# Kernel tuning notes

Measured on AMD Instinct MI355X. Metric: run time of the kernel, lower is better.

The kernel has to match this reference:

```python
import jax, jax.numpy as jnp
import numpy as np

EPS = 1e-7

def _sample_project(feat, pid, w1, b1, w2, b2):
    # feat: [B, C, H, W]; pid: [P] flat spatial indices into H*W
    B, C, H, W = feat.shape
    fr = jnp.transpose(feat, (0, 2, 3, 1)).reshape(B, H * W, C)  # [B, HW, C]
    x = fr[:, pid, :].reshape(B * pid.shape[0], C)               # gather -> [B*P, C]
    x = jnp.maximum(x @ w1 + b1, 0.0) @ w2 + b2                  # 2-layer MLP
    norm = jnp.sqrt(jnp.sum(x * x, axis=1, keepdims=True))       # L2 over channels
    return x / (norm + EPS)


def setup_inputs() -> dict:
    key = jax.random.key(0)
    ks = jax.random.split(key, 16)
    NC = 256
    shapes = [(16, 256, 128, 128), (16, 512, 64, 64), (16, 1024, 32, 32)]
    inp = {}
    for i, s in enumerate(shapes):
        inp[f"feat{i}"] = jax.random.normal(ks[i], s, dtype=jnp.float32)
        hw = s[2] * s[3]
        inp[f"patch_id{i}"] = jax.random.randint(ks[3 + i], (256,), 0, hw, dtype=jnp.int64)
        C = s[1]
        g = 0.02  # init_gain (normal init)
        inp[f"w1_{i}"] = g * jax.random.normal(ks[6 + 3 * i], (C, NC), dtype=jnp.float32)
        inp[f"b1_{i}"] = jnp.zeros((NC,), dtype=jnp.float32)
        inp[f"w2_{i}"] = g * jax.random.normal(ks[7 + 3 * i], (NC, NC), dtype=jnp.float32)
        inp[f"b2_{i}"] = jnp.zeros((NC,), dtype=jnp.float32)
    return inp


def reference(feat0, feat1, feat2, patch_id0, patch_id1, patch_id2,
              w1_0, b1_0, w2_0, b2_0,
              w1_1, b1_1, w2_1, b2_1,
              w1_2, b1_2, w2_2, b2_2):
    out0 = _sample_project(feat0, patch_id0, w1_0, b1_0, w2_0, b2_0)
    out1 = _sample_project(feat1, patch_id1, w1_1, b1_1, w2_1, b2_1)
    out2 = _sample_project(feat2, patch_id2, w1_2, b1_2, w2_2, b2_2)
    return (out0, out1, out2)
```

## Files before the change

### kernel.cpp

```cpp
#include <hip/hip_runtime.h>

typedef __attribute__((ext_vector_type(8))) short short8;
typedef __attribute__((ext_vector_type(4))) float floatx4;
typedef __attribute__((ext_vector_type(4))) unsigned int uintx4;

__device__ __forceinline__ short f2bf(float f) {
    unsigned u = __builtin_bit_cast(unsigned, f);
    u = (u + 0x7FFFu + ((u >> 16) & 1u)) >> 16;
    return (short)u;
}


__global__ __launch_bounds__(256) void sort_pid(
    const int* __restrict__ pid0, const int* __restrict__ pid1, const int* __restrict__ pid2,
    unsigned short* __restrict__ wsb)
{
    __shared__ int ks[256];
    __shared__ int vs[256];
    const int* pid = (blockIdx.x == 0) ? pid0 : (blockIdx.x == 1) ? pid1 : pid2;
    int t = threadIdx.x;
    ks[t] = pid[t];
    vs[t] = t;
    __syncthreads();
    for (int k = 2; k <= 256; k <<= 1) {
        for (int j = k >> 1; j > 0; j >>= 1) {
            int ixj = t ^ j;
            if (ixj > t) {
                int a = ks[t], b = ks[ixj];
                bool asc = ((t & k) == 0);
                if (asc ? (a > b) : (a < b)) {
                    ks[t] = b; ks[ixj] = a;
                    int va = vs[t]; vs[t] = vs[ixj]; vs[ixj] = va;
                }
            }
            __syncthreads();
        }
    }
    int2* sp = (int2*)(wsb + 7995392) + blockIdx.x * 256;
    sp[t] = make_int2(ks[t], vs[t]);
}

__global__ __launch_bounds__(256) void gather_prep(
    const float* __restrict__ feat0, const float* __restrict__ feat1, const float* __restrict__ feat2,
    const float* __restrict__ w10, const float* __restrict__ w11, const float* __restrict__ w12,
    const float* __restrict__ w20, const float* __restrict__ w21, const float* __restrict__ w22,
    unsigned short* __restrict__ wsb)
{
    __shared__ float tile[32][33];
    int blk = blockIdx.x;
    int t = threadIdx.x;

    if (blk < 640) {
        const float* in; unsigned short* out; int K, t0;
        if (blk < 64)       { in = w10; out = wsb;          K = 256;  t0 = 0; }
        else if (blk < 192) { in = w11; out = wsb + 65536;  K = 512;  t0 = 64; }
        else if (blk < 448) { in = w12; out = wsb + 196608; K = 1024; t0 = 192; }
        else if (blk < 512) { in = w20; out = wsb + 458752; K = 256;  t0 = 448; }
        else if (blk < 576) { in = w21; out = wsb + 524288; K = 256;  t0 = 512; }
        else                { in = w22; out = wsb + 589824; K = 256;  t0 = 576; }
        int tile_id = blk - t0;
        int tk = K >> 5;
        int k0 = (tile_id % tk) << 5;
        int n0 = (tile_id / tk) << 5;
        int j = t & 31, i0 = (t >> 5) << 2;
        #pragma unroll
        for (int u = 0; u < 4; u++)
            tile[i0 + u][j] = in[(size_t)(k0 + i0 + u) * 256 + (n0 + j)];
        __syncthreads();
        int kf = t & 31, nf0 = (t >> 5) << 2;
        #pragma unroll
        for (int u = 0; u < 4; u++)
            out[(size_t)(n0 + nf0 + u) * K + (k0 + kf)] = (unsigned short)f2bf(tile[kf][nf0 + u]);
        return;
    }

    blk -= 640;
    const float* feat; const int2* sp; unsigned short* xg;
    int lblk, cl8, HW, n;
    const int2* spb = (const int2*)(wsb + 7995392);
    if (blk < 512)       { feat = feat0; sp = spb;       lblk = blk;        cl8 = 5; HW = 16384; n = 512;  xg = wsb + 655360; }
    else if (blk < 1536) { feat = feat1; sp = spb + 256; lblk = blk - 512;  cl8 = 6; HW = 4096;  n = 1024; xg = wsb + 1703936; }
    else                 { feat = feat2; sp = spb + 512; lblk = blk - 1536; cl8 = 7; HW = 1024;  n = 2048; xg = wsb + 3801088; }

    lblk = (lblk & 7) * (n >> 3) + (lblk >> 3);

    int g   = (lblk << 8) + t;
    int row = g >> cl8;
    int gk  = (g & ((1 << cl8) - 1)) << 3;
    int b = row >> 8, pp = row & 255;
    int2 e = sp[pp];
    int s = e.x, op = e.y;
    int C = 8 << cl8;

    const float* gp = feat + (size_t)b * ((size_t)C * HW) + (size_t)gk * HW + s;
    float v[8];
    #pragma unroll
    for (int j = 0; j < 8; j++) v[j] = gp[(size_t)j * HW];
    short8 sv;
    #pragma unroll
    for (int j = 0; j < 8; j++) sv[j] = f2bf(v[j]);
    *(short8*)(xg + (size_t)(b * 256 + op) * C + gk) = sv;
}

__global__ __launch_bounds__(256, 2) void fused_mlp(
    const float* __restrict__ b1_0, const float* __restrict__ b1_1, const float* __restrict__ b1_2,
    const float* __restrict__ b2_0, const float* __restrict__ b2_1, const float* __restrict__ b2_2,
    const unsigned short* __restrict__ wsb,
    float* __restrict__ out)
{
    __shared__ __align__(16) unsigned short smem[26944];
    unsigned short* wsS = smem;
    unsigned short* xs  = smem + 18432;
    unsigned short* hs  = smem + 18432;
    float* rs = (float*)(smem + 26880);

    int blk = blockIdx.x;
    int scale = 2 - (blk >> 7);
    int mblk = blk & 127;

    const float* b1; const float* b2;
    const unsigned short* w1T; const unsigned short* w2T; const unsigned short* xg;
    int C; size_t outBase;
    if (scale == 0) { b1 = b1_0; b2 = b2_0; w1T = wsb;          w2T = wsb + 458752;
                      xg = wsb + 655360;  C = 256;  outBase = 0; }
    else if (scale == 1) { b1 = b1_1; b2 = b2_1; w1T = wsb + 65536;  w2T = wsb + 524288;
                      xg = wsb + 1703936; C = 512;  outBase = 1048576; }
    else            { b1 = b1_2; b2 = b2_2; w1T = wsb + 196608; w2T = wsb + 589824;
                      xg = wsb + 3801088; C = 1024; outBase = 2097152; }

    int t = threadIdx.x;
    int wid = t >> 6, lane = t & 63, quad = lane >> 4, l15 = lane & 15;
    int r0 = (wid & 1) << 4;
    int c0 = (wid >> 1) << 7;

    int gr = t >> 3;
    int gk = (t & 7) << 3;
    int row_g = (mblk << 5) + gr;
    const unsigned short* xrow = xg + (size_t)row_g * C;

    floatx4 acc[8];
    #pragma unroll
    for (int f = 0; f < 8; f++) acc[f] = (floatx4){0.f, 0.f, 0.f, 0.f};

    for (int kc = 0; kc < C; kc += 64) {
        *(short8*)(xs + gr * 72 + gk) = *(const short8*)(xrow + kc + gk);
        {
            const uintx4* src = (const uintx4*)(w1T + (size_t)t * C + kc);
            uintx4* dst = (uintx4*)(wsS + t * 72);
            #pragma unroll
            for (int j2 = 0; j2 < 8; j2++) dst[j2] = src[j2];
        }
        __syncthreads();
        const unsigned short* aRow = xs + (r0 + l15) * 72;
        const unsigned short* bRow = wsS + (c0 + l15) * 72;
        #pragma unroll
        for (int ks = 0; ks < 2; ks++) {
            short8 af = *(const short8*)(aRow + ks * 32 + quad * 8);
            #pragma unroll
            for (int f = 0; f < 8; f++) {
                short8 bf = *(const short8*)(bRow + f * (16 * 72) + ks * 32 + quad * 8);
                acc[f] = __builtin_amdgcn_mfma_f32_16x16x32_bf16(af, bf, acc[f], 0, 0, 0);
            }
        }
        __syncthreads();
    }

    {
        float bias1[8];
        #pragma unroll
        for (int f = 0; f < 8; f++) bias1[f] = b1[c0 + f * 16 + l15];
        #pragma unroll
        for (int f = 0; f < 8; f++)
            #pragma unroll
            for (int reg = 0; reg < 4; reg++) {
                float h = fmaxf(acc[f][reg] + bias1[f], 0.f);
                hs[(r0 + quad * 4 + reg) * 264 + (c0 + f * 16 + l15)] = (unsigned short)f2bf(h);
            }
    }

    #pragma unroll
    for (int f = 0; f < 8; f++) acc[f] = (floatx4){0.f, 0.f, 0.f, 0.f};
    const unsigned short* hA = hs + (r0 + l15) * 264;
    for (int kc = 0; kc < 256; kc += 64) {
        {
            const uintx4* src = (const uintx4*)(w2T + (size_t)t * 256 + kc);
            uintx4* dst = (uintx4*)(wsS + t * 72);
            #pragma unroll
            for (int j2 = 0; j2 < 8; j2++) dst[j2] = src[j2];
        }
        __syncthreads();
        const unsigned short* bRow = wsS + (c0 + l15) * 72;
        #pragma unroll
        for (int ks = 0; ks < 2; ks++) {
            short8 af = *(const short8*)(hA + kc + ks * 32 + quad * 8);
            #pragma unroll
            for (int f = 0; f < 8; f++) {
                short8 bf = *(const short8*)(bRow + f * (16 * 72) + ks * 32 + quad * 8);
                acc[f] = __builtin_amdgcn_mfma_f32_16x16x32_bf16(af, bf, acc[f], 0, 0, 0);
            }
        }
        __syncthreads();
    }

    {
        float bias2[8];
        #pragma unroll
        for (int f = 0; f < 8; f++) bias2[f] = b2[c0 + f * 16 + l15];
        float psq[4] = {0.f, 0.f, 0.f, 0.f};
        #pragma unroll
        for (int f = 0; f < 8; f++)
            #pragma unroll
            for (int reg = 0; reg < 4; reg++) {
                float yv = acc[f][reg] + bias2[f];
                acc[f][reg] = yv;
                psq[reg] += yv * yv;
            }
        #pragma unroll
        for (int m = 1; m < 16; m <<= 1)
            #pragma unroll
            for (int reg = 0; reg < 4; reg++)
                psq[reg] += __shfl_xor(psq[reg], m, 16);

        if (t < 32) rs[t] = 0.f;
        __syncthreads();
        if (l15 == 0) {
            #pragma unroll
            for (int reg = 0; reg < 4; reg++)
                atomicAdd(&rs[r0 + quad * 4 + reg], psq[reg]);
        }
        __syncthreads();

        #pragma unroll
        for (int f = 0; f < 8; f++)
            #pragma unroll
            for (int reg = 0; reg < 4; reg++) {
                int row = r0 + quad * 4 + reg;
                float inv = 1.f / (sqrtf(rs[row]) + 1e-7f);
                out[outBase + (size_t)((mblk << 5) + row) * 256 + (c0 + f * 16 + l15)] =
                    acc[f][reg] * inv;
            }
    }
}

extern "C" void kernel_launch(void* const* d_in, const int* in_sizes, int n_in,
                              void* d_out, int out_size, void* d_ws, size_t ws_size,
                              hipStream_t stream)
{
    (void)n_in; (void)out_size; (void)ws_size;
    bool dict = (in_sizes[1] == 256);
    const float *feat[3], *w1[3], *b1[3], *w2[3], *b2[3];
    const int* pid[3];
    for (int i = 0; i < 3; i++) {
        if (dict) {
            feat[i] = (const float*)d_in[i * 6 + 0];
            pid[i]  = (const int*)  d_in[i * 6 + 1];
            w1[i]   = (const float*)d_in[i * 6 + 2];
            b1[i]   = (const float*)d_in[i * 6 + 3];
            w2[i]   = (const float*)d_in[i * 6 + 4];
            b2[i]   = (const float*)d_in[i * 6 + 5];
        } else {
            feat[i] = (const float*)d_in[i];
            pid[i]  = (const int*)  d_in[3 + i];
            w1[i]   = (const float*)d_in[6 + 4 * i + 0];
            b1[i]   = (const float*)d_in[6 + 4 * i + 1];
            w2[i]   = (const float*)d_in[6 + 4 * i + 2];
            b2[i]   = (const float*)d_in[6 + 4 * i + 3];
        }
    }
    unsigned short* wsb = (unsigned short*)d_ws;
    sort_pid<<<3, 256, 0, stream>>>(pid[0], pid[1], pid[2], wsb);
    gather_prep<<<4224, 256, 0, stream>>>(feat[0], feat[1], feat[2],
                                          w1[0], w1[1], w1[2],
                                          w2[0], w2[1], w2[2], wsb);
    fused_mlp<<<384, 256, 0, stream>>>(b1[0], b1[1], b1[2],
                                       b2[0], b2[1], b2[2],
                                       wsb, (float*)d_out);
}
```

Measured before the change: 533.0 us.

## Restructure feature gather to use sorted-patch coalescing and LDS transpose

Reworks the gather stage so each block handles one batch and a 64-channel group. Lanes read consecutive sorted patch positions within each channel plane, and the results are staged as bf16 in a shared-memory tile. The tile is then transposed and written out as contiguous 16-byte row chunks. The aim is better locality on the strided NCHW gather: sorted indices bring nearby spatial reads together and each block reuses its index set. In exchange there are far fewer blocks, a larger shared-memory footprint, and an extra barrier.

New measurement: 521.9 us. 2.1% less time.

```diff
diff --git a/kernel.cpp b/kernel.cpp
--- a/kernel.cpp
+++ b/kernel.cpp
@@ -40,17 +40,59 @@
     sp[t] = make_int2(ks[t], vs[t]);
 }
 
+template<int NCH>
+__device__ __forceinline__ void gather_body(
+    const float* __restrict__ featb, const int2* __restrict__ sp,
+    unsigned short* __restrict__ xg, int C, int HW, int b, int cg, int sh,
+    unsigned short (*tile)[256], int t)
+{
+    int wid = t >> 6, lane = t & 63;
+    int s0 = sh * 128;
+    int sj[NCH];
+    #pragma unroll
+    for (int j = 0; j < NCH; ++j) sj[j] = sp[s0 + j * 64 + lane].x;
+
+    int cbase = cg * 64 + wid * 16;
+    #pragma unroll 2
+    for (int cl = 0; cl < 16; ++cl) {
+        const float* plane = featb + (size_t)(cbase + cl) * HW;
+        float v[NCH];
+        #pragma unroll
+        for (int j = 0; j < NCH; ++j) v[j] = plane[sj[j]];
+        #pragma unroll
+        for (int j = 0; j < NCH; ++j)
+            tile[wid * 16 + cl][j * 64 + lane] = (unsigned short)f2bf(v[j]);
+    }
+    __syncthreads();
+    if (t < NCH * 64) {
+        int2 e = sp[s0 + t];
+        int row = b * 256 + e.y;
+        short8 rv[8];
+        #pragma unroll
+        for (int c8 = 0; c8 < 8; ++c8)
+            #pragma unroll
+            for (int k = 0; k < 8; ++k)
+                rv[c8][k] = (short)tile[c8 * 8 + k][t];
+        unsigned short* dst = xg + (size_t)row * C + cg * 64;
+        #pragma unroll
+        for (int c8 = 0; c8 < 8; ++c8)
+            *(short8*)(dst + c8 * 8) = rv[c8];
+    }
+}
+
 __global__ __launch_bounds__(256) void gather_prep(
     const float* __restrict__ feat0, const float* __restrict__ feat1, const float* __restrict__ feat2,
     const float* __restrict__ w10, const float* __restrict__ w11, const float* __restrict__ w12,
     const float* __restrict__ w20, const float* __restrict__ w21, const float* __restrict__ w22,
     unsigned short* __restrict__ wsb)
 {
-    __shared__ float tile[32][33];
+    __shared__ unsigned short tile[64][256];
+    __shared__ float wt[32][33];
     int blk = blockIdx.x;
     int t = threadIdx.x;
 
-    if (blk < 640) {
+    if (blk >= 512) {
+        blk -= 512;
         const float* in; unsigned short* out; int K, t0;
         if (blk < 64)       { in = w10; out = wsb;          K = 256;  t0 = 0; }
         else if (blk < 192) { in = w11; out = wsb + 65536;  K = 512;  t0 = 64; }
@@ -65,41 +107,29 @@
         int j = t & 31, i0 = (t >> 5) << 2;
         #pragma unroll
         for (int u = 0; u < 4; u++)
-            tile[i0 + u][j] = in[(size_t)(k0 + i0 + u) * 256 + (n0 + j)];
+            wt[i0 + u][j] = in[(size_t)(k0 + i0 + u) * 256 + (n0 + j)];
         __syncthreads();
         int kf = t & 31, nf0 = (t >> 5) << 2;
         #pragma unroll
         for (int u = 0; u < 4; u++)
-            out[(size_t)(n0 + nf0 + u) * K + (k0 + kf)] = (unsigned short)f2bf(tile[kf][nf0 + u]);
+            out[(size_t)(n0 + nf0 + u) * K + (k0 + kf)] = (unsigned short)f2bf(wt[kf][nf0 + u]);
         return;
     }
 
-    blk -= 640;
-    const float* feat; const int2* sp; unsigned short* xg;
-    int lblk, cl8, HW, n;
     const int2* spb = (const int2*)(wsb + 7995392);
-    if (blk < 512)       { feat = feat0; sp = spb;       lblk = blk;        cl8 = 5; HW = 16384; n = 512;  xg = wsb + 655360; }
-    else if (blk < 1536) { feat = feat1; sp = spb + 256; lblk = blk - 512;  cl8 = 6; HW = 4096;  n = 1024; xg = wsb + 1703936; }
-    else                 { feat = feat2; sp = spb + 512; lblk = blk - 1536; cl8 = 7; HW = 1024;  n = 2048; xg = wsb + 3801088; }
-
-    lblk = (lblk & 7) * (n >> 3) + (lblk >> 3);
-
-    int g   = (lblk << 8) + t;
-    int row = g >> cl8;
-    int gk  = (g & ((1 << cl8) - 1)) << 3;
-    int b = row >> 8, pp = row & 255;
-    int2 e = sp[pp];
-    int s = e.x, op = e.y;
-    int C = 8 << cl8;
-
-    const float* gp = feat + (size_t)b * ((size_t)C * HW) + (size_t)gk * HW + s;
-    float v[8];
-    #pragma unroll
-    for (int j = 0; j < 8; j++) v[j] = gp[(size_t)j * HW];
-    short8 sv;
-    #pragma unroll
-    for (int j = 0; j < 8; j++) sv[j] = f2bf(v[j]);
-    *(short8*)(xg + (size_t)(b * 256 + op) * C + gk) = sv;
+    if (blk < 128) {
+        int b = blk >> 3, r = blk & 7, cg = r >> 1, sh = r & 1;
+        const float* featb = feat0 + (size_t)b * 256 * 16384;
+        gather_body<2>(featb, spb, wsb + 655360, 256, 16384, b, cg, sh, tile, t);
+    } else if (blk < 256) {
+        int l = blk - 128, b = l >> 3, cg = l & 7;
+        const float* featb = feat1 + (size_t)b * 512 * 4096;
+        gather_body<4>(featb, spb + 256, wsb + 1703936, 512, 4096, b, cg, 0, tile, t);
+    } else {
+        int l = blk - 256, b = l >> 4, cg = l & 15;
+        const float* featb = feat2 + (size_t)b * 1024 * 1024;
+        gather_body<4>(featb, spb + 512, wsb + 3801088, 1024, 1024, b, cg, 0, tile, t);
+    }
 }
 
 __global__ __launch_bounds__(256, 2) void fused_mlp(
@@ -269,7 +299,7 @@
     }
     unsigned short* wsb = (unsigned short*)d_ws;
     sort_pid<<<3, 256, 0, stream>>>(pid[0], pid[1], pid[2], wsb);
-    gather_prep<<<4224, 256, 0, stream>>>(feat[0], feat[1], feat[2],
+    gather_prep<<<1152, 256, 0, stream>>>(feat[0], feat[1], feat[2],
                                           w1[0], w1[1], w1[2],
                                           w2[0], w2[1], w2[2], wsb);
     fused_mlp<<<384, 256, 0, stream>>>(b1[0], b1[1], b1[2],
```

## Stream full feature planes with coalesced float4 reads for dense gather scales

Applied to the files above, without the earlier changes.

For scales 1 and 2, where 256 random pixels per batch hit most cache lines of the small planes, the gather now reads every plane with coalesced float4 loads instead of scattered 4-byte loads. Each thread uses a bucket table computed in sort_pid by binary search over sorted patch ids to pick out matching pixels into a shared-memory tile, which is then written as bf16 rows. Scale 0 keeps a point gather, now with 16 channels per thread, and the launch shrinks to 1408 blocks. This trades more bytes read from DRAM for better coalescing and fewer memory transactions, and adds a serial inner loop per bucket.

Result: slower. 635.1 us (+19.1%).

```diff
diff --git a/kernel.cpp b/kernel.cpp
--- a/kernel.cpp
+++ b/kernel.cpp
@@ -38,6 +38,54 @@
     }
     int2* sp = (int2*)(wsb + 7995392) + blockIdx.x * 256;
     sp[t] = make_int2(ks[t], vs[t]);
+
+    if (blockIdx.x >= 1) {
+        int W = (blockIdx.x == 1) ? 1024 : 256;
+        int* jst = (int*)(wsb + 7998464) + ((blockIdx.x == 2) ? 1040 : 0);
+        for (int w = t; w <= W; w += 256) {
+            int target = w * 4;
+            int lo = 0, hi = 256;
+            while (lo < hi) { int mid = (lo + hi) >> 1; if (ks[mid] < target) lo = mid + 1; else hi = mid; }
+            jst[w] = lo;
+        }
+    }
+}
+
+template<int CH, int IT, int HW>
+__device__ __forceinline__ void stream_gather(
+    const float* __restrict__ featb, const int2* __restrict__ sp, const int* __restrict__ jst,
+    unsigned short* __restrict__ xg, int C, int b, int cg,
+    unsigned short* tileRaw, int t)
+{
+    unsigned short (*tile)[256] = (unsigned short (*)[256])tileRaw;
+    int cbase = cg * CH;
+    #pragma unroll
+    for (int it = 0; it < IT; ++it) {
+        int w = it * 256 + t;
+        int js = jst[w], je = jst[w + 1];
+        int pos = w * 4;
+        #pragma unroll 8
+        for (int c = 0; c < CH; ++c) {
+            const float* plane = featb + (size_t)(cbase + c) * HW;
+            float4 v = ((const float4*)plane)[w];
+            for (int j = js; j < je; ++j) {
+                int s = sp[j].x - pos;
+                float val = (s & 2) ? ((s & 1) ? v.w : v.z) : ((s & 1) ? v.y : v.x);
+                tile[c][j] = (unsigned short)f2bf(val);
+            }
+        }
+    }
+    __syncthreads();
+    int2 e = sp[t];
+    int row = b * 256 + e.y;
+    unsigned short* dst = xg + (size_t)row * C + cbase;
+    #pragma unroll
+    for (int c8 = 0; c8 < CH / 8; ++c8) {
+        short8 rv;
+        #pragma unroll
+        for (int k = 0; k < 8; ++k) rv[k] = (short)tile[c8 * 8 + k][t];
+        *(short8*)(dst + c8 * 8) = rv;
+    }
 }
 
 __global__ __launch_bounds__(256) void gather_prep(
@@ -46,60 +94,68 @@
     const float* __restrict__ w20, const float* __restrict__ w21, const float* __restrict__ w22,
     unsigned short* __restrict__ wsb)
 {
-    __shared__ float tile[32][33];
+    __shared__ __align__(16) unsigned char smemRaw[32768];
     int blk = blockIdx.x;
     int t = threadIdx.x;
-
-    if (blk < 640) {
-        const float* in; unsigned short* out; int K, t0;
-        if (blk < 64)       { in = w10; out = wsb;          K = 256;  t0 = 0; }
-        else if (blk < 192) { in = w11; out = wsb + 65536;  K = 512;  t0 = 64; }
-        else if (blk < 448) { in = w12; out = wsb + 196608; K = 1024; t0 = 192; }
-        else if (blk < 512) { in = w20; out = wsb + 458752; K = 256;  t0 = 448; }
-        else if (blk < 576) { in = w21; out = wsb + 524288; K = 256;  t0 = 512; }
-        else                { in = w22; out = wsb + 589824; K = 256;  t0 = 576; }
-        int tile_id = blk - t0;
-        int tk = K >> 5;
-        int k0 = (tile_id % tk) << 5;
-        int n0 = (tile_id / tk) << 5;
-        int j = t & 31, i0 = (t >> 5) << 2;
-        #pragma unroll
-        for (int u = 0; u < 4; u++)
-            tile[i0 + u][j] = in[(size_t)(k0 + i0 + u) * 256 + (n0 + j)];
-        __syncthreads();
-        int kf = t & 31, nf0 = (t >> 5) << 2;
-        #pragma unroll
-        for (int u = 0; u < 4; u++)
-            out[(size_t)(n0 + nf0 + u) * K + (k0 + kf)] = (unsigned short)f2bf(tile[kf][nf0 + u]);
+    const int2* spb = (const int2*)(wsb + 7995392);
+    const int* jstb = (const int*)(wsb + 7998464);
+
+    if (blk < 256) {
+        int b = blk >> 4, cg = blk & 15;
+        const float* featb = feat1 + (size_t)b * 512 * 4096;
+        stream_gather<32, 4, 4096>(featb, spb + 256, jstb, wsb + 1703936, 512, b, cg,
+                                   (unsigned short*)smemRaw, t);
         return;
     }
-
-    blk -= 640;
-    const float* feat; const int2* sp; unsigned short* xg;
-    int lblk, cl8, HW, n;
-    const int2* spb = (const int2*)(wsb + 7995392);
-    if (blk < 512)       { feat = feat0; sp = spb;       lblk = blk;        cl8 = 5; HW = 16384; n = 512;  xg = wsb + 655360; }
-    else if (blk < 1536) { feat = feat1; sp = spb + 256; lblk = blk - 512;  cl8 = 6; HW = 4096;  n = 1024; xg = wsb + 1703936; }
-    else                 { feat = feat2; sp = spb + 512; lblk = blk - 1536; cl8 = 7; HW = 1024;  n = 2048; xg = wsb + 3801088; }
-
-    lblk = (lblk & 7) * (n >> 3) + (lblk >> 3);
-
-    int g   = (lblk << 8) + t;
-    int row = g >> cl8;
-    int gk  = (g & ((1 << cl8) - 1)) << 3;
-    int b = row >> 8, pp = row & 255;
-    int2 e = sp[pp];
-    int s = e.x, op = e.y;
-    int C = 8 << cl8;
-
-    const float* gp = feat + (size_t)b * ((size_t)C * HW) + (size_t)gk * HW + s;
-    float v[8];
-    #pragma unroll
-    for (int j = 0; j < 8; j++) v[j] = gp[(size_t)j * HW];
-    short8 sv;
-    #pragma unroll
-    for (int j = 0; j < 8; j++) sv[j] = f2bf(v[j]);
-    *(short8*)(xg + (size_t)(b * 256 + op) * C + gk) = sv;
+    if (blk < 512) {
+        int l = blk - 256;
+        int j = l * 16 + (t >> 4);
+        int chunk16 = t & 15;
+        int b = j >> 8;
+        int2 e = spb[j & 255];
+        const float* gp = feat0 + (size_t)b * 256 * 16384 + (size_t)(chunk16 * 16) * 16384 + e.x;
+        float v[16];
+        #pragma unroll
+        for (int k = 0; k < 16; ++k) v[k] = gp[(size_t)k * 16384];
+        int orow = b * 256 + e.y;
+        unsigned short* dst = wsb + 655360 + (size_t)orow * 256 + chunk16 * 16;
+        short8 s0, s1;
+        #pragma unroll
+        for (int k = 0; k < 8; ++k) { s0[k] = f2bf(v[k]); s1[k] = f2bf(v[8 + k]); }
+        *(short8*)dst = s0;
+        *(short8*)(dst + 8) = s1;
+        return;
+    }
+    if (blk < 768) {
+        int l = blk - 512, b = l >> 4, cg = l & 15;
+        const float* featb = feat2 + (size_t)b * 1024 * 1024;
+        stream_gather<64, 1, 1024>(featb, spb + 512, jstb + 1040, wsb + 3801088, 1024, b, cg,
+                                   (unsigned short*)smemRaw, t);
+        return;
+    }
+
+    blk -= 768;
+    float (*wt)[33] = (float (*)[33])smemRaw;
+    const float* in; unsigned short* out; int K, t0;
+    if (blk < 64)       { in = w10; out = wsb;          K = 256;  t0 = 0; }
+    else if (blk < 192) { in = w11; out = wsb + 65536;  K = 512;  t0 = 64; }
+    else if (blk < 448) { in = w12; out = wsb + 196608; K = 1024; t0 = 192; }
+    else if (blk < 512) { in = w20; out = wsb + 458752; K = 256;  t0 = 448; }
+    else if (blk < 576) { in = w21; out = wsb + 524288; K = 256;  t0 = 512; }
+    else                { in = w22; out = wsb + 589824; K = 256;  t0 = 576; }
+    int tile_id = blk - t0;
+    int tk = K >> 5;
+    int k0 = (tile_id % tk) << 5;
+    int n0 = (tile_id / tk) << 5;
+    int j = t & 31, i0 = (t >> 5) << 2;
+    #pragma unroll
+    for (int u = 0; u < 4; u++)
+        wt[i0 + u][j] = in[(size_t)(k0 + i0 + u) * 256 + (n0 + j)];
+    __syncthreads();
+    int kf = t & 31, nf0 = (t >> 5) << 2;
+    #pragma unroll
+    for (int u = 0; u < 4; u++)
+        out[(size_t)(n0 + nf0 + u) * K + (k0 + kf)] = (unsigned short)f2bf(wt[kf][nf0 + u]);
 }
 
 __global__ __launch_bounds__(256, 2) void fused_mlp(
@@ -269,7 +325,7 @@
     }
     unsigned short* wsb = (unsigned short*)d_ws;
     sort_pid<<<3, 256, 0, stream>>>(pid[0], pid[1], pid[2], wsb);
-    gather_prep<<<4224, 256, 0, stream>>>(feat[0], feat[1], feat[2],
+    gather_prep<<<1408, 256, 0, stream>>>(feat[0], feat[1], feat[2],
                                           w1[0], w1[1], w1[2],
                                           w2[0], w2[1], w2[2], wsb);
     fused_mlp<<<384, 256, 0, stream>>>(b1[0], b1[1], b1[2],
```
